# Kernel optimization log

Measured on AMD Instinct MI355X. Metric: run time of the kernel, lower is better.

Reference implementation:

```python
import jax, jax.numpy as jnp
import numpy as np

LEAK = 0.3          # config['leak_rate']
LAST_N = 8          # config['last_n_outputs']


def setup_inputs() -> dict:
    key = jax.random.key(0)
    k1, k2, k3, k4, k5 = jax.random.split(key, 5)
    B, T, F, H, O = 256, 1000, 64, 1024, 10
    x = jax.random.normal(k1, (B, T, F), dtype=jnp.float32)
    w_in = jax.random.normal(k2, (F, H), dtype=jnp.float32) * 0.2
    # reservoir matrix scaled to spectral radius ~0.9 (randn HxH has radius ~sqrt(H))
    w_r = jax.random.normal(k3, (H, H), dtype=jnp.float32) * (0.9 / np.sqrt(H))
    w_lin = jax.random.normal(k4, (O, H * LAST_N), dtype=jnp.float32) * 0.02
    b_lin = jax.random.normal(k5, (O,), dtype=jnp.float32) * 0.02
    return {"x": x, "w_in": w_in, "w_r": w_r, "w_lin": w_lin, "b_lin": b_lin}


def _esn_forward(x, w_in, w_r, w_lin, b_lin):
    B, T, F = x.shape
    H = w_in.shape[1]
    n = LAST_N
    # t = 0: h_0 = h_hat (no leaky combine per original code)
    h = jnp.tanh(x[:, 0, :] @ w_in)

    def step(h, xt):
        h_hat = jnp.tanh(xt @ w_in + h @ w_r)
        return (1.0 - LEAK) * h + LEAK * h_hat

    # steps 1 .. T-n-1: carry only, no outputs stored
    def body_nohist(h, xt):
        return step(h, xt), None

    xs_mid = jnp.swapaxes(x[:, 1:T - n, :], 0, 1)   # [T-n-1, B, F]
    h, _ = jax.lax.scan(body_nohist, h, xs_mid)

    # steps T-n .. T-1: keep states (out_list in original)
    def body_hist(h, xt):
        h = step(h, xt)
        return h, h

    xs_tail = jnp.swapaxes(x[:, T - n:, :], 0, 1)   # [n, B, F]
    _, hs = jax.lax.scan(body_hist, h, xs_tail)     # [n, B, H]

    # torch.cat(out_list, dim=1): oldest kept state first -> [B, n*H]
    feats = jnp.transpose(hs, (1, 0, 2)).reshape(B, n * H)
    return feats @ w_lin.T + b_lin


def reference(x, w_in, w_r, w_lin, b_lin):
    return _esn_forward(x, w_in, w_r, w_lin, b_lin)
```

## Files before the change

### kernel.cpp

```cpp
#include <hip/hip_runtime.h>
#include <math.h>

#define LEAK   0.3f
#define ONEML  0.7f

typedef unsigned short u16;
typedef unsigned int   u32;
typedef unsigned long long u64;
typedef __attribute__((ext_vector_type(4))) float f32x4;
typedef __attribute__((ext_vector_type(8))) short s16x8;

constexpr int B = 256, T = 1000, F = 64, H = 1024, O = 10, NTAIL = 8;
constexpr int TSTART  = T - NTAIL;
constexpr int KS      = 34;
constexpr int PSTRIDE = 1096;


constexpr size_t OFF_PACKED = 0;
constexpr size_t OFF_HGL    = 0x220000;
constexpr size_t OFF_FEATS  = 0x420000;

__device__ __forceinline__ u16 f2bf(float f) {
  union { float f; u32 u; } v; v.f = f;
  u32 r = v.u + 0x7fffu + ((v.u >> 16) & 1u);
  return (u16)(r >> 16);
}

__device__ __forceinline__ float ftanh(float s) {
  const float sc = fminf(fmaxf(s, -9.0f), 9.0f);
  const float e2 = __builtin_amdgcn_exp2f(sc * 2.8853900817779268f);
  return 1.0f - 2.0f * __builtin_amdgcn_rcpf(e2 + 1.0f);
}

__global__ void esn_pack(const float* __restrict__ w_in, const float* __restrict__ w_r,
                         u16* __restrict__ packed) {
  int gid = blockIdx.x * 256 + threadIdx.x;
  if (gid >= 64 * KS * 64) return;
  int lane = gid & 63;
  int ks   = (gid >> 6) % KS;
  int nt   = gid / (KS * 64);
  int n    = nt * 16 + (lane & 15);
  int g    = lane >> 4;
  u16 v[8];
  #pragma unroll
  for (int jj = 0; jj < 8; ++jj) {
    int kk = 8 * g + jj;
    float w;
    if (ks < 2) w = w_in[(ks * 32 + kk) * H + n];
    else        w = w_r[((ks - 2) * 32 + kk) * H + n];
    v[jj] = f2bf(w);
  }
  u64* dst = (u64*)(packed + (size_t)gid * 8);
  dst[0] = ((const u64*)v)[0];
  dst[1] = ((const u64*)v)[1];
}

__global__ __launch_bounds__(512, 1) void esn_recur(const float* __restrict__ x,
    const u16* __restrict__ packed, u32* __restrict__ hgl, float* __restrict__ feats) {
  __shared__ u16 panel[2][16][PSTRIDE];
  __shared__ u16 forcepad[6144];

  const int tid  = threadIdx.x;
  const int lane = tid & 63, wv = tid >> 6;
  const int ci   = blockIdx.x >> 3;
  const int cj   = blockIdx.x & 7;
  const int g    = lane >> 4, m16 = lane & 15;
  const int nt   = cj * 8 + wv;
  const int cc   = nt * 16 + m16;
  const int bbase = ci * 16;
  const bool ownCols = ((tid >> 6) == cj);

  s16x8 bfrag[KS];
  #pragma unroll
  for (int ks = 0; ks < KS; ++ks)
    bfrag[ks] = *(const s16x8*)(packed + (((size_t)nt * KS + ks) * 64 + lane) * 8);

  float hreg[4] = {0.f, 0.f, 0.f, 0.f};

  for (int t = 0; t < T; ++t) {
    const int buf = t & 1;
    const int nb  = buf ^ 1;

    {
      const int r = tid >> 5;
      const int c = (tid & 31) * 2;
      const float2 v = *(const float2*)(x + (((size_t)(bbase + r)) * T + t) * (size_t)F + c);
      u16 o[2] = { f2bf(v.x), f2bf(v.y) };
      *(u32*)&panel[buf][r][c] = *(const u32*)o;
    }

    if (t == 0) {
      #pragma unroll
      for (int it = 0; it < 16; ++it)
        *(u32*)&panel[buf][it][64 + tid * 2] = 0u;
    } else {
      const u32 st = (u32)t;
      const int pb = (t + 1) & 1;
      const u32* base = hgl + (((size_t)pb * 16 + ci) * 16) * H + tid * 2;
      u64 vb[16];
      int guard = 0;
      for (;;) {
        bool ok = true;
        if (!ownCols) {
          #pragma unroll
          for (int it = 0; it < 16; ++it)
            vb[it] = __hip_atomic_load((const u64*)(base + (size_t)it * H),
                                       __ATOMIC_RELAXED, __HIP_MEMORY_SCOPE_AGENT);
          #pragma unroll
          for (int it = 0; it < 16; ++it)
            ok &= ((((u32)vb[it]) & 0xffffu) == st) &&
                  ((((u32)(vb[it] >> 32)) & 0xffffu) == st);
        }
        if (__all((int)ok)) break;
        if (++guard > 4096) break;
      }
      if (!ownCols) {
        #pragma unroll
        for (int it = 0; it < 16; ++it) {
          u16 o[2] = { (u16)(((u32)vb[it]) >> 16), (u16)(((u32)(vb[it] >> 32)) >> 16) };
          *(u32*)&panel[buf][it][64 + tid * 2] = *(const u32*)o;
        }
      }
      asm volatile("" ::: "memory");
    }
    __syncthreads();

    f32x4 acc0 = {0.f,0.f,0.f,0.f}, acc1 = {0.f,0.f,0.f,0.f};
    #pragma unroll
    for (int ks = 0; ks < KS; ++ks) {
      s16x8 a = *(const s16x8*)&panel[buf][m16][ks * 32 + g * 8];
      if (ks & 1) acc1 = __builtin_amdgcn_mfma_f32_16x16x32_bf16(a, bfrag[ks], acc1, 0, 0, 0);
      else        acc0 = __builtin_amdgcn_mfma_f32_16x16x32_bf16(a, bfrag[ks], acc0, 0, 0, 0);
    }

    #pragma unroll
    for (int r = 0; r < 4; ++r) {
      const float s  = acc0[r] + acc1[r];
      const float th = ftanh(s);
      const float hn = (t == 0) ? th : (ONEML * hreg[r] + LEAK * th);
      hreg[r] = hn;
      const int rr = g * 4 + r;
      panel[nb][rr][64 + cc] = f2bf(hn);
      if (t >= TSTART)
        feats[((size_t)(bbase + rr)) * (H * NTAIL) + (t - TSTART) * H + cc] = hn;
    }

    asm volatile("s_waitcnt lgkmcnt(0)" ::: "memory");
    {
      const int r  = lane >> 2;
      const int c4 = (lane & 3) * 4;
      const u64 two = *(const u64*)&panel[nb][r][64 + nt * 16 + c4];
      const u32 st  = (u32)(t + 1);
      const u32 w0 = (((u32)(two       & 0xffffu)) << 16) | st;
      const u32 w1 = (((u32)((two>>16) & 0xffffu)) << 16) | st;
      const u32 w2 = (((u32)((two>>32) & 0xffffu)) << 16) | st;
      const u32 w3 = (((u32)((two>>48) & 0xffffu)) << 16) | st;
      u32* gp = hgl + (((size_t)buf * 16 + ci) * 16 + r) * H + nt * 16 + c4;
      __hip_atomic_store((u64*)gp,       (((u64)w1) << 32) | w0,
                         __ATOMIC_RELAXED, __HIP_MEMORY_SCOPE_AGENT);
      __hip_atomic_store((u64*)(gp + 2), (((u64)w3) << 32) | w2,
                         __ATOMIC_RELAXED, __HIP_MEMORY_SCOPE_AGENT);
    }
  }
  if (tid == 511) ((volatile u16*)forcepad)[0] = (u16)lane;
}

__global__ __launch_bounds__(256) void esn_out(const float* __restrict__ feats,
    const float* __restrict__ w_lin, const float* __restrict__ b_lin,
    float* __restrict__ out) {
  const int b = blockIdx.x;
  const int tid = threadIdx.x;
  const int lane = tid & 63, wv = tid >> 6;
  float p[O];
  #pragma unroll
  for (int o = 0; o < O; ++o) p[o] = 0.f;
  const float* fr = feats + (size_t)b * (H * NTAIL);
  for (int idx = tid; idx < H * NTAIL; idx += 256) {
    const float f = fr[idx];
    #pragma unroll
    for (int o = 0; o < O; ++o) p[o] += f * w_lin[o * (H * NTAIL) + idx];
  }
  __shared__ float red[O][4];
  #pragma unroll
  for (int o = 0; o < O; ++o) {
    float v = p[o];
    for (int off = 32; off > 0; off >>= 1) v += __shfl_down(v, off);
    if (lane == 0) red[o][wv] = v;
  }
  __syncthreads();
  if (tid < O)
    out[b * O + tid] = red[tid][0] + red[tid][1] + red[tid][2] + red[tid][3] + b_lin[tid];
}

extern "C" void kernel_launch(void* const* d_in, const int* in_sizes, int n_in,
                              void* d_out, int out_size, void* d_ws, size_t ws_size,
                              hipStream_t stream) {
  const float* x     = (const float*)d_in[0];
  const float* w_in  = (const float*)d_in[1];
  const float* w_r   = (const float*)d_in[2];
  const float* w_lin = (const float*)d_in[3];
  const float* b_lin = (const float*)d_in[4];
  char* ws = (char*)d_ws;
  u16* packed = (u16*)(ws + OFF_PACKED);
  u32* hgl    = (u32*)(ws + OFF_HGL);
  float* feats= (float*)(ws + OFF_FEATS);
  float* out  = (float*)d_out;

  esn_pack<<<(64 * KS * 64 + 255) / 256, 256, 0, stream>>>(w_in, w_r, packed);

  void* args[] = { (void*)&x, (void*)&packed, (void*)&hgl, (void*)&feats };
  hipLaunchCooperativeKernel((void*)esn_recur, dim3(128), dim3(512), args, 0, stream);

  esn_out<<<B, 256, 0, stream>>>(feats, w_lin, b_lin, out);
}
```

Measured before the change: 4.064 ms.

## Add per-wave progress flags and triple-buffer hidden state exchange

Adds a per-cluster flag array that each wave bumps after publishing its slice, so consumers first spin on one small flag word per lane instead of repeatedly polling all 16 rows of tagged hidden state. The global hidden-state exchange moves from double to triple buffering, which lets fast producers run one step further ahead without overwriting data still being read. The data poll now retries only the rows still pending. This adds a memset and an extra store plus a flag spin each step, and the flag store is relaxed with no release ordering, so the per-element tag check is still what guarantees correctness.

New measurement: 4.135 ms. About the same (+1.8%).

```diff
diff --git a/kernel.cpp b/kernel.cpp
--- a/kernel.cpp
+++ b/kernel.cpp
@@ -18,7 +18,8 @@
 
 constexpr size_t OFF_PACKED = 0;
 constexpr size_t OFF_HGL    = 0x220000;
-constexpr size_t OFF_FEATS  = 0x420000;
+constexpr size_t OFF_FLAGS  = 0x520000;
+constexpr size_t OFF_FEATS  = 0x524000;
 
 __device__ __forceinline__ u16 f2bf(float f) {
   union { float f; u32 u; } v; v.f = f;
@@ -56,7 +57,8 @@
 }
 
 __global__ __launch_bounds__(512, 1) void esn_recur(const float* __restrict__ x,
-    const u16* __restrict__ packed, u32* __restrict__ hgl, float* __restrict__ feats) {
+    const u16* __restrict__ packed, u32* __restrict__ hgl,
+    u16* __restrict__ flags, float* __restrict__ feats) {
   __shared__ u16 panel[2][16][PSTRIDE];
   __shared__ u16 forcepad[6144];
 
@@ -78,8 +80,10 @@
   float hreg[4] = {0.f, 0.f, 0.f, 0.f};
 
   for (int t = 0; t < T; ++t) {
-    const int buf = t & 1;
-    const int nb  = buf ^ 1;
+    const int buf   = t & 1;
+    const int nb    = buf ^ 1;
+    const int wslot = t % 3;
+    const int rslot = (t + 2) % 3;
 
     {
       const int r = tid >> 5;
@@ -89,37 +93,55 @@
       *(u32*)&panel[buf][r][c] = *(const u32*)o;
     }
 
+    if (t > 0) {
+      const u16 target = (u16)t;
+      const u16* fp = flags + ci * 64 + lane;
+      int guard = 0;
+      for (;;) {
+        u16 fv = __hip_atomic_load(fp, __ATOMIC_RELAXED, __HIP_MEMORY_SCOPE_AGENT);
+        if (__all((int)(fv >= target))) break;
+        if (++guard > (1 << 16)) break;
+      }
+      asm volatile("" ::: "memory");
+    }
+
     if (t == 0) {
       #pragma unroll
       for (int it = 0; it < 16; ++it)
         *(u32*)&panel[buf][it][64 + tid * 2] = 0u;
-    } else {
+    } else if (!ownCols) {
       const u32 st = (u32)t;
-      const int pb = (t + 1) & 1;
-      const u32* base = hgl + (((size_t)pb * 16 + ci) * 16) * H + tid * 2;
+      const u32* base = hgl + (((size_t)rslot * 16 + ci) * 16) * H + tid * 2;
       u64 vb[16];
+      #pragma unroll
+      for (int it = 0; it < 16; ++it)
+        vb[it] = __hip_atomic_load((const u64*)(base + (size_t)it * H),
+                                   __ATOMIC_RELAXED, __HIP_MEMORY_SCOPE_AGENT);
+      u32 pending = 0;
+      #pragma unroll
+      for (int it = 0; it < 16; ++it) {
+        const bool good = ((((u32)vb[it]) & 0xffffu) == st) &&
+                          ((((u32)(vb[it] >> 32)) & 0xffffu) == st);
+        pending |= (good ? 0u : 1u) << it;
+      }
       int guard = 0;
-      for (;;) {
-        bool ok = true;
-        if (!ownCols) {
-          #pragma unroll
-          for (int it = 0; it < 16; ++it)
-            vb[it] = __hip_atomic_load((const u64*)(base + (size_t)it * H),
-                                       __ATOMIC_RELAXED, __HIP_MEMORY_SCOPE_AGENT);
-          #pragma unroll
-          for (int it = 0; it < 16; ++it)
-            ok &= ((((u32)vb[it]) & 0xffffu) == st) &&
-                  ((((u32)(vb[it] >> 32)) & 0xffffu) == st);
-        }
-        if (__all((int)ok)) break;
-        if (++guard > 4096) break;
-      }
-      if (!ownCols) {
+      while (pending && ++guard <= 4096) {
         #pragma unroll
         for (int it = 0; it < 16; ++it) {
-          u16 o[2] = { (u16)(((u32)vb[it]) >> 16), (u16)(((u32)(vb[it] >> 32)) >> 16) };
-          *(u32*)&panel[buf][it][64 + tid * 2] = *(const u32*)o;
+          if (pending & (1u << it)) {
+            const u64 v = __hip_atomic_load((const u64*)(base + (size_t)it * H),
+                                            __ATOMIC_RELAXED, __HIP_MEMORY_SCOPE_AGENT);
+            if (((((u32)v) & 0xffffu) == st) && ((((u32)(v >> 32)) & 0xffffu) == st) ) {
+              vb[it] = v;
+              pending &= ~(1u << it);
+            }
+          }
         }
+      }
+      #pragma unroll
+      for (int it = 0; it < 16; ++it) {
+        u16 o[2] = { (u16)(((u32)vb[it]) >> 16), (u16)(vb[it] >> 48) };
+        *(u32*)&panel[buf][it][64 + tid * 2] = *(const u32*)o;
       }
       asm volatile("" ::: "memory");
     }
@@ -151,16 +173,19 @@
       const int c4 = (lane & 3) * 4;
       const u64 two = *(const u64*)&panel[nb][r][64 + nt * 16 + c4];
       const u32 st  = (u32)(t + 1);
-      const u32 w0 = (((u32)(two       & 0xffffu)) << 16) | st;
-      const u32 w1 = (((u32)((two>>16) & 0xffffu)) << 16) | st;
-      const u32 w2 = (((u32)((two>>32) & 0xffffu)) << 16) | st;
-      const u32 w3 = (((u32)((two>>48) & 0xffffu)) << 16) | st;
-      u32* gp = hgl + (((size_t)buf * 16 + ci) * 16 + r) * H + nt * 16 + c4;
+      const u32 w0 = (((u32)(two        & 0xffffu)) << 16) | st;
+      const u32 w1 = (((u32)((two>>16)  & 0xffffu)) << 16) | st;
+      const u32 w2 = (((u32)((two>>32)  & 0xffffu)) << 16) | st;
+      const u32 w3 = (((u32)((two>>48)  & 0xffffu)) << 16) | st;
+      u32* gp = hgl + (((size_t)wslot * 16 + ci) * 16 + r) * H + nt * 16 + c4;
       __hip_atomic_store((u64*)gp,       (((u64)w1) << 32) | w0,
                          __ATOMIC_RELAXED, __HIP_MEMORY_SCOPE_AGENT);
       __hip_atomic_store((u64*)(gp + 2), (((u64)w3) << 32) | w2,
                          __ATOMIC_RELAXED, __HIP_MEMORY_SCOPE_AGENT);
     }
+    if (lane == 0)
+      __hip_atomic_store(&flags[ci * 64 + nt], (u16)(t + 1),
+                         __ATOMIC_RELAXED, __HIP_MEMORY_SCOPE_AGENT);
   }
   if (tid == 511) ((volatile u16*)forcepad)[0] = (u16)lane;
 }
@@ -203,12 +228,14 @@
   char* ws = (char*)d_ws;
   u16* packed = (u16*)(ws + OFF_PACKED);
   u32* hgl    = (u32*)(ws + OFF_HGL);
+  u16* flags  = (u16*)(ws + OFF_FLAGS);
   float* feats= (float*)(ws + OFF_FEATS);
   float* out  = (float*)d_out;
 
+  hipMemsetAsync(flags, 0, 4096, stream);
   esn_pack<<<(64 * KS * 64 + 255) / 256, 256, 0, stream>>>(w_in, w_r, packed);
 
-  void* args[] = { (void*)&x, (void*)&packed, (void*)&hgl, (void*)&feats };
+  void* args[] = { (void*)&x, (void*)&packed, (void*)&hgl, (void*)&flags, (void*)&feats };
   hipLaunchCooperativeKernel((void*)esn_recur, dim3(128), dim3(512), args, 0, stream);
 
   esn_out<<<B, 256, 0, stream>>>(feats, w_lin, b_lin, out);
```
